# Kernel tuning notes

Hardware: AMD Instinct MI355X
Metric: run time of the kernel (lower is better)

Reference implementation:

```python
import jax, jax.numpy as jnp
import numpy as np

IMG_FEAT = 2048
HIDDEN = 512


def setup_inputs() -> dict:
    key = jax.random.key(0)
    ks = jax.random.split(key, 9)
    B, R = 512, 10
    img = jax.random.normal(ks[0], (B * R, IMG_FEAT), dtype=jnp.float32)
    ques = jax.random.normal(ks[1], (B * R, HIDDEN), dtype=jnp.float32)
    hist = jax.random.normal(ks[2], (B * R, R, HIDDEN), dtype=jnp.float32)
    fusion = IMG_FEAT + HIDDEN
    # kaiming-uniform-ish init scales
    W_fuse = jax.random.uniform(ks[3], (HIDDEN, fusion), dtype=jnp.float32,
                                minval=-1.0, maxval=1.0) * np.sqrt(6.0 / fusion)
    b_fuse = jnp.zeros((HIDDEN,), dtype=jnp.float32)
    w_att = jax.random.uniform(ks[4], (HIDDEN,), dtype=jnp.float32,
                               minval=-1.0, maxval=1.0) * np.sqrt(6.0 / HIDDEN)
    b_att = jnp.zeros((), dtype=jnp.float32)
    W_hist = jax.random.uniform(ks[5], (HIDDEN, HIDDEN), dtype=jnp.float32,
                                minval=-1.0, maxval=1.0) * np.sqrt(6.0 / HIDDEN)
    b_hist = jnp.zeros((HIDDEN,), dtype=jnp.float32)
    return {
        "img": img, "ques": ques, "hist": hist,
        "W_fuse": W_fuse, "b_fuse": b_fuse,
        "w_att": w_att, "b_att": b_att,
        "W_hist": W_hist, "b_hist": b_hist,
        "batch_size": B, "num_rounds": R,
    }


def reference(img, ques, hist, W_fuse, b_fuse, w_att, b_att, W_hist, b_hist,
              batch_size, num_rounds):
    # Dropout is identity (eval mode).
    BR = batch_size * num_rounds
    # fused embedding: tanh(Linear(cat(img, ques)))  -> [B*R, D]
    fused_vec = jnp.concatenate([img, ques], axis=1)
    fused = jnp.tanh(fused_vec @ W_fuse.T + b_fuse)
    D = fused.shape[-1]
    hist_r = hist.reshape(BR, num_rounds, D)  # [B*R, R, D]
    # scores: (hist * broadcast(fused)) @ w_att + b_att  -> [B*R, R]
    # equivalent to the repeat + elementwise-mul + linear-to-scalar in torch
    scores = jnp.einsum('brd,bd,d->br', hist_r, fused, w_att) + b_att
    attn = jax.nn.softmax(scores, axis=1)  # softmax over num_rounds
    hist_embed = jnp.einsum('br,brd->bd', attn, hist_r)  # weighted sum
    hist_embed = jnp.tanh(hist_embed @ W_hist.T + b_hist)
    out = fused + hist_embed
    return out.reshape(batch_size, num_rounds, D)
```

## Files before the change

kernel.cpp:

```cpp
#include <hip/hip_runtime.h>
#include <hip/hip_bf16.h>

#define HIDDEN 512
#define IMGF   2048
#define RNDS   10

typedef float  f32x4  __attribute__((ext_vector_type(4)));
typedef __bf16 bf16x8 __attribute__((ext_vector_type(8)));
typedef unsigned short u16x8 __attribute__((ext_vector_type(8)));

__device__ __forceinline__ unsigned short f2bf(float x) {
    union { float f; unsigned u; } v; v.f = x;
    unsigned r = v.u + 0x7FFFu + ((v.u >> 16) & 1u);
    return (unsigned short)(r >> 16);
}
__device__ __forceinline__ float bf2f(unsigned short h) {
    union { unsigned u; float f; } v; v.u = ((unsigned)h) << 16;
    return v.f;
}

__device__ __forceinline__ void cp16_async(const void* g, void* l) {
    __builtin_amdgcn_global_load_lds(
        (const __attribute__((address_space(1))) unsigned int*)g,
        (__attribute__((address_space(3))) unsigned int*)l,
        16, 0, 0);
}

__global__ __launch_bounds__(256)
void cvt_bf16(const float* __restrict__ p0, long n0,
              const float* __restrict__ p1, long n1,
              const float* __restrict__ p2, long n2,
              const float* __restrict__ p3, long n3,
              unsigned short* __restrict__ q0, unsigned short* __restrict__ q1,
              unsigned short* __restrict__ q2, unsigned short* __restrict__ q3)
{
    long i = ((long)blockIdx.x * 256 + threadIdx.x) * 4;
    const float* s; unsigned short* d; long j;
    if      (i < n0)            { s = p0; d = q0; j = i; }
    else if (i < n0 + n1)       { s = p1; d = q1; j = i - n0; }
    else if (i < n0 + n1 + n2)  { s = p2; d = q2; j = i - n0 - n1; }
    else                        { s = p3; d = q3; j = i - n0 - n1 - n2; }
    float4 v = *(const float4*)(s + j);
    ushort4 o;
    o.x = f2bf(v.x); o.y = f2bf(v.y); o.z = f2bf(v.z); o.w = f2bf(v.w);
    *(ushort4*)(d + j) = o;
}

template<bool RESID>
__global__ __launch_bounds__(256, 4)
void gemm_bt_tanh(const unsigned short* __restrict__ A0, int lda0,
                  const unsigned short* __restrict__ A1, int lda1, int kSplit,
                  const unsigned short* __restrict__ W,
                  const float* __restrict__ bias,
                  const unsigned short* __restrict__ residb,
                  float* __restrict__ outf, unsigned short* __restrict__ outb,
                  int K)
{
    __shared__ unsigned short lA[2][32 * 64];
    __shared__ unsigned short lB[2][64 * 64];

    const int bm = blockIdx.x * 32;
    const int bn = blockIdx.y * 64;
    const int t    = threadIdx.x;
    const int lane = t & 63;
    const int wave = t >> 6;
    const int wm = (wave >> 1) * 16;
    const int wn = (wave & 1) * 32;
    const int lr = lane & 15;
    const int lq = lane >> 4;

    const unsigned short* Wb0 = W + (size_t)bn * K;

    auto stage_tiles = [&](int kt, int buf) {
        int k0 = kt << 6;
        const unsigned short* Ab; int lda;
        if (k0 < kSplit) { Ab = A0 + (size_t)bm * lda0 + k0;            lda = lda0; }
        else             { Ab = A1 + (size_t)bm * lda1 + (k0 - kSplit); lda = lda1; }
        {
            int r = t >> 3, s = (t & 7) ^ (r & 7);
            cp16_async(Ab + (size_t)r * lda + s * 8, &lA[buf][t * 8]);
        }
        #pragma unroll
        for (int h = 0; h < 2; ++h) {
            int ci = h * 256 + t;
            int r = ci >> 3, s = (ci & 7) ^ (r & 7);
            cp16_async(Wb0 + k0 + (size_t)r * K + s * 8, &lB[buf][ci * 8]);
        }
    };

    f32x4 acc[2] = {};
    const int NT = K >> 6;

    stage_tiles(0, 0);
    for (int kt = 0; kt < NT; ++kt) {
        __syncthreads();
        if (kt + 1 < NT) stage_tiles(kt + 1, (kt + 1) & 1);
        const unsigned short* a = &lA[kt & 1][0];
        const unsigned short* b = &lB[kt & 1][0];
        #pragma unroll
        for (int kh = 0; kh < 2; ++kh) {
            const int c = kh * 4 + lq;
            const int ra = wm + lr;
            bf16x8 af = __builtin_bit_cast(bf16x8,
                *(const u16x8*)&a[ra * 64 + ((c ^ (ra & 7)) * 8)]);
            #pragma unroll
            for (int ni = 0; ni < 2; ++ni) {
                const int rb = wn + ni * 16 + lr;
                bf16x8 bf = __builtin_bit_cast(bf16x8,
                    *(const u16x8*)&b[rb * 64 + ((c ^ (rb & 7)) * 8)]);
                acc[ni] = __builtin_amdgcn_mfma_f32_16x16x32_bf16(
                    af, bf, acc[ni], 0, 0, 0);
            }
        }
    }

    #pragma unroll
    for (int ni = 0; ni < 2; ++ni) {
        const int col = bn + wn + ni * 16 + lr;
        const float bc = bias[col];
        const int rbase = bm + wm + lq * 4;
        #pragma unroll
        for (int j = 0; j < 4; ++j) {
            const size_t idx = (size_t)(rbase + j) * HIDDEN + col;
            float v = tanhf(acc[ni][j] + bc);
            if (RESID) outf[idx] = v + bf2f(residb[idx]);
            else       outb[idx] = f2bf(v);
        }
    }
}

__global__ __launch_bounds__(256)
void attn_embed(const float* __restrict__ hist,
                const unsigned short* __restrict__ fusedb,
                const float* __restrict__ w_att,
                const float* __restrict__ b_att,
                unsigned short* __restrict__ hembed)
{
    const int lane = threadIdx.x & 63;
    const int wave = threadIdx.x >> 6;
    const int b = blockIdx.x * 4 + wave;
    const int d = lane * 8;

    float g[8];
    {
        u16x8 f = *(const u16x8*)(fusedb + (size_t)b * HIDDEN + d);
        const float4 w0 = *(const float4*)(w_att + d);
        const float4 w1 = *(const float4*)(w_att + d + 4);
        g[0]=bf2f(f[0])*w0.x; g[1]=bf2f(f[1])*w0.y; g[2]=bf2f(f[2])*w0.z; g[3]=bf2f(f[3])*w0.w;
        g[4]=bf2f(f[4])*w1.x; g[5]=bf2f(f[5])*w1.y; g[6]=bf2f(f[6])*w1.z; g[7]=bf2f(f[7])*w1.w;
    }
    const float* hb = hist + (size_t)b * RNDS * HIDDEN + d;

    float h[RNDS][8], p[RNDS];
    #pragma unroll
    for (int r = 0; r < RNDS; ++r) {
        const float4 a0 = *(const float4*)(hb + r * HIDDEN);
        const float4 a1 = *(const float4*)(hb + r * HIDDEN + 4);
        h[r][0]=a0.x; h[r][1]=a0.y; h[r][2]=a0.z; h[r][3]=a0.w;
        h[r][4]=a1.x; h[r][5]=a1.y; h[r][6]=a1.z; h[r][7]=a1.w;
        float s = 0.f;
        #pragma unroll
        for (int i = 0; i < 8; ++i) s += h[r][i] * g[i];
        p[r] = s;
    }
    #pragma unroll
    for (int r = 0; r < RNDS; ++r)
        #pragma unroll
        for (int m = 1; m < 64; m <<= 1)
            p[r] += __shfl_xor(p[r], m, 64);

    const float ba = b_att[0];
    float mx = -1e30f;
    #pragma unroll
    for (int r = 0; r < RNDS; ++r) mx = fmaxf(mx, p[r] + ba);
    float sum = 0.f, a[RNDS];
    #pragma unroll
    for (int r = 0; r < RNDS; ++r) { a[r] = __expf(p[r] + ba - mx); sum += a[r]; }
    const float inv = 1.0f / sum;

    float e[8] = {};
    #pragma unroll
    for (int r = 0; r < RNDS; ++r)
        #pragma unroll
        for (int i = 0; i < 8; ++i) e[i] += a[r] * h[r][i];

    ushort4 o0, o1;
    o0.x=f2bf(e[0]*inv); o0.y=f2bf(e[1]*inv); o0.z=f2bf(e[2]*inv); o0.w=f2bf(e[3]*inv);
    o1.x=f2bf(e[4]*inv); o1.y=f2bf(e[5]*inv); o1.z=f2bf(e[6]*inv); o1.w=f2bf(e[7]*inv);
    unsigned short* q = hembed + (size_t)b * HIDDEN + d;
    *(ushort4*)q = o0;
    *(ushort4*)(q + 4) = o1;
}

extern "C" void kernel_launch(void* const* d_in, const int* in_sizes, int n_in,
                              void* d_out, int out_size, void* d_ws, size_t ws_size,
                              hipStream_t stream)
{
    const float* img    = (const float*)d_in[0];
    const float* ques   = (const float*)d_in[1];
    const float* hist   = (const float*)d_in[2];
    const float* W_fuse = (const float*)d_in[3];
    const float* b_fuse = (const float*)d_in[4];
    const float* w_att  = (const float*)d_in[5];
    const float* b_att  = (const float*)d_in[6];
    const float* W_hist = (const float*)d_in[7];
    const float* b_hist = (const float*)d_in[8];

    const long n_img  = in_sizes[0];
    const long n_ques = in_sizes[1];
    const long n_Wf   = in_sizes[3];
    const long n_Wh   = in_sizes[7];
    const int  BR     = (int)(n_ques / HIDDEN);

    unsigned short* imgb   = (unsigned short*)d_ws;
    unsigned short* quesb  = imgb   + n_img;
    unsigned short* Wfb    = quesb  + n_ques;
    unsigned short* Whb    = Wfb    + n_Wf;
    unsigned short* fusedb = Whb    + n_Wh;
    unsigned short* hembb  = fusedb + (size_t)BR * HIDDEN;

    const long total4 = (n_img + n_ques + n_Wf + n_Wh) / 4;
    cvt_bf16<<<dim3((unsigned)((total4 + 255) / 256)), dim3(256), 0, stream>>>(
        img, n_img, ques, n_ques, W_fuse, n_Wf, W_hist, n_Wh,
        imgb, quesb, Wfb, Whb);

    dim3 blk(256);
    dim3 g1(BR / 32, HIDDEN / 64);

    gemm_bt_tanh<false><<<g1, blk, 0, stream>>>(
        imgb, IMGF, quesb, HIDDEN, IMGF,
        Wfb, b_fuse, nullptr, nullptr, fusedb, IMGF + HIDDEN);

    attn_embed<<<dim3(BR / 4), blk, 0, stream>>>(hist, fusedb, w_att, b_att, hembb);

    gemm_bt_tanh<true><<<g1, blk, 0, stream>>>(
        hembb, HIDDEN, nullptr, 0, HIDDEN,
        Whb, b_hist, fusedb, (float*)d_out, nullptr, HIDDEN);
}
```

Baseline: 257.0 us.

## Convert activations to bf16 inside GEMM and enlarge tiles with grouped block order

Stops pre-converting img and ques to bf16 in a separate pass. The first GEMM now reads fp32 activations straight from global memory into registers and packs them to bf16 there, with only the weights staged through LDS. Both GEMMs move to 64x64 tiles on 128-thread blocks, with each wave computing 32x64 and a grouped block index intended to improve L2 reuse. This removes a full fp32 read and bf16 write of the activations, but the A operand is now loaded uncached from global per wave, and each block reads it again for every N tile.

```diff
diff --git a/kernel.cpp b/kernel.cpp
--- a/kernel.cpp
+++ b/kernel.cpp
@@ -26,105 +26,184 @@
         16, 0, 0);
 }
 
+__device__ __forceinline__ bf16x8 pack8(float4 p0, float4 p1) {
+    union { bf16x8 v; __hip_bfloat162 h[4]; } u;
+    u.h[0] = __float22bfloat162_rn(make_float2(p0.x, p0.y));
+    u.h[1] = __float22bfloat162_rn(make_float2(p0.z, p0.w));
+    u.h[2] = __float22bfloat162_rn(make_float2(p1.x, p1.y));
+    u.h[3] = __float22bfloat162_rn(make_float2(p1.z, p1.w));
+    return u.v;
+}
+
 __global__ __launch_bounds__(256)
 void cvt_bf16(const float* __restrict__ p0, long n0,
               const float* __restrict__ p1, long n1,
-              const float* __restrict__ p2, long n2,
-              const float* __restrict__ p3, long n3,
-              unsigned short* __restrict__ q0, unsigned short* __restrict__ q1,
-              unsigned short* __restrict__ q2, unsigned short* __restrict__ q3)
+              unsigned short* __restrict__ q0, unsigned short* __restrict__ q1)
 {
     long i = ((long)blockIdx.x * 256 + threadIdx.x) * 4;
     const float* s; unsigned short* d; long j;
-    if      (i < n0)            { s = p0; d = q0; j = i; }
-    else if (i < n0 + n1)       { s = p1; d = q1; j = i - n0; }
-    else if (i < n0 + n1 + n2)  { s = p2; d = q2; j = i - n0 - n1; }
-    else                        { s = p3; d = q3; j = i - n0 - n1 - n2; }
+    if (i < n0) { s = p0; d = q0; j = i; }
+    else        { s = p1; d = q1; j = i - n0; }
     float4 v = *(const float4*)(s + j);
     ushort4 o;
     o.x = f2bf(v.x); o.y = f2bf(v.y); o.z = f2bf(v.z); o.w = f2bf(v.w);
     *(ushort4*)(d + j) = o;
 }
 
-template<bool RESID>
-__global__ __launch_bounds__(256, 4)
-void gemm_bt_tanh(const unsigned short* __restrict__ A0, int lda0,
-                  const unsigned short* __restrict__ A1, int lda1, int kSplit,
-                  const unsigned short* __restrict__ W,
-                  const float* __restrict__ bias,
-                  const unsigned short* __restrict__ residb,
-                  float* __restrict__ outf, unsigned short* __restrict__ outb,
-                  int K)
-{
-    __shared__ unsigned short lA[2][32 * 64];
+__global__ __launch_bounds__(128, 4)
+void gemm1(const float* __restrict__ A0,
+           const float* __restrict__ A1,
+           const unsigned short* __restrict__ W,
+           const float* __restrict__ bias,
+           unsigned short* __restrict__ outb)
+{
     __shared__ unsigned short lB[2][64 * 64];
-
-    const int bm = blockIdx.x * 32;
-    const int bn = blockIdx.y * 64;
+    const int id = blockIdx.x;
+    const int bm = ((id >> 6) * 8 + (id & 7)) * 64;
+    const int bn = ((id >> 3) & 7) * 64;
     const int t    = threadIdx.x;
     const int lane = t & 63;
-    const int wave = t >> 6;
-    const int wm = (wave >> 1) * 16;
-    const int wn = (wave & 1) * 32;
+    const int wv   = t >> 6;
     const int lr = lane & 15;
     const int lq = lane >> 4;
+    const int K = IMGF + HIDDEN;
 
     const unsigned short* Wb0 = W + (size_t)bn * K;
-
-    auto stage_tiles = [&](int kt, int buf) {
+    auto stageB = [&](int kt, int buf) {
         int k0 = kt << 6;
-        const unsigned short* Ab; int lda;
-        if (k0 < kSplit) { Ab = A0 + (size_t)bm * lda0 + k0;            lda = lda0; }
-        else             { Ab = A1 + (size_t)bm * lda1 + (k0 - kSplit); lda = lda1; }
-        {
-            int r = t >> 3, s = (t & 7) ^ (r & 7);
-            cp16_async(Ab + (size_t)r * lda + s * 8, &lA[buf][t * 8]);
-        }
-        #pragma unroll
-        for (int h = 0; h < 2; ++h) {
-            int ci = h * 256 + t;
+        #pragma unroll
+        for (int h = 0; h < 4; ++h) {
+            int ci = h * 128 + t;
             int r = ci >> 3, s = (ci & 7) ^ (r & 7);
             cp16_async(Wb0 + k0 + (size_t)r * K + s * 8, &lB[buf][ci * 8]);
         }
     };
 
-    f32x4 acc[2] = {};
+    const int row0 = bm + wv * 32 + lr;
+    const int row1 = row0 + 16;
+
+    f32x4 acc[2][4] = {};
     const int NT = K >> 6;
 
-    stage_tiles(0, 0);
+    stageB(0, 0);
     for (int kt = 0; kt < NT; ++kt) {
         __syncthreads();
-        if (kt + 1 < NT) stage_tiles(kt + 1, (kt + 1) & 1);
-        const unsigned short* a = &lA[kt & 1][0];
+        if (kt + 1 < NT) stageB(kt + 1, (kt + 1) & 1);
         const unsigned short* b = &lB[kt & 1][0];
+        const int k0 = kt << 6;
+        const float* Ab; int lda, ko;
+        if (k0 < IMGF) { Ab = A0; lda = IMGF;   ko = k0; }
+        else           { Ab = A1; lda = HIDDEN; ko = k0 - IMGF; }
         #pragma unroll
         for (int kh = 0; kh < 2; ++kh) {
-            const int c = kh * 4 + lq;
-            const int ra = wm + lr;
-            bf16x8 af = __builtin_bit_cast(bf16x8,
-                *(const u16x8*)&a[ra * 64 + ((c ^ (ra & 7)) * 8)]);
+            const int kf = ko + kh * 32 + lq * 8;
+            const float* r0p = Ab + (size_t)row0 * lda + kf;
+            const float* r1p = Ab + (size_t)row1 * lda + kf;
+            bf16x8 af[2];
+            af[0] = pack8(*(const float4*)r0p, *(const float4*)(r0p + 4));
+            af[1] = pack8(*(const float4*)r1p, *(const float4*)(r1p + 4));
             #pragma unroll
-            for (int ni = 0; ni < 2; ++ni) {
-                const int rb = wn + ni * 16 + lr;
-                bf16x8 bf = __builtin_bit_cast(bf16x8,
+            for (int ni = 0; ni < 4; ++ni) {
+                const int rb = ni * 16 + lr;
+                const int c  = kh * 4 + lq;
+                bf16x8 bfr = __builtin_bit_cast(bf16x8,
                     *(const u16x8*)&b[rb * 64 + ((c ^ (rb & 7)) * 8)]);
-                acc[ni] = __builtin_amdgcn_mfma_f32_16x16x32_bf16(
-                    af, bf, acc[ni], 0, 0, 0);
+                #pragma unroll
+                for (int mi = 0; mi < 2; ++mi)
+                    acc[mi][ni] = __builtin_amdgcn_mfma_f32_16x16x32_bf16(
+                        af[mi], bfr, acc[mi][ni], 0, 0, 0);
             }
         }
     }
 
     #pragma unroll
-    for (int ni = 0; ni < 2; ++ni) {
-        const int col = bn + wn + ni * 16 + lr;
+    for (int ni = 0; ni < 4; ++ni) {
+        const int col = bn + ni * 16 + lr;
         const float bc = bias[col];
-        const int rbase = bm + wm + lq * 4;
-        #pragma unroll
-        for (int j = 0; j < 4; ++j) {
-            const size_t idx = (size_t)(rbase + j) * HIDDEN + col;
-            float v = tanhf(acc[ni][j] + bc);
-            if (RESID) outf[idx] = v + bf2f(residb[idx]);
-            else       outb[idx] = f2bf(v);
+        #pragma unroll
+        for (int mi = 0; mi < 2; ++mi) {
+            const int rbase = bm + wv * 32 + mi * 16 + lq * 4;
+            #pragma unroll
+            for (int j = 0; j < 4; ++j)
+                outb[(size_t)(rbase + j) * HIDDEN + col] =
+                    f2bf(tanhf(acc[mi][ni][j] + bc));
+        }
+    }
+}
+
+__global__ __launch_bounds__(128, 4)
+void gemm2(const unsigned short* __restrict__ A,
+           const unsigned short* __restrict__ W,
+           const float* __restrict__ bias,
+           const unsigned short* __restrict__ residb,
+           float* __restrict__ outf)
+{
+    __shared__ unsigned short lB[2][64 * 64];
+    const int id = blockIdx.x;
+    const int bm = ((id >> 6) * 8 + (id & 7)) * 64;
+    const int bn = ((id >> 3) & 7) * 64;
+    const int t    = threadIdx.x;
+    const int lane = t & 63;
+    const int wv   = t >> 6;
+    const int lr = lane & 15;
+    const int lq = lane >> 4;
+    const int K = HIDDEN;
+
+    const unsigned short* Wb0 = W + (size_t)bn * K;
+    auto stageB = [&](int kt, int buf) {
+        int k0 = kt << 6;
+        #pragma unroll
+        for (int h = 0; h < 4; ++h) {
+            int ci = h * 128 + t;
+            int r = ci >> 3, s = (ci & 7) ^ (r & 7);
+            cp16_async(Wb0 + k0 + (size_t)r * K + s * 8, &lB[buf][ci * 8]);
+        }
+    };
+
+    const int row0 = bm + wv * 32 + lr;
+    const int row1 = row0 + 16;
+
+    f32x4 acc[2][4] = {};
+    const int NT = K >> 6;
+
+    stageB(0, 0);
+    for (int kt = 0; kt < NT; ++kt) {
+        __syncthreads();
+        if (kt + 1 < NT) stageB(kt + 1, (kt + 1) & 1);
+        const unsigned short* b = &lB[kt & 1][0];
+        const int k0 = kt << 6;
+        #pragma unroll
+        for (int kh = 0; kh < 2; ++kh) {
+            const int kf = k0 + kh * 32 + lq * 8;
+            bf16x8 af[2];
+            af[0] = __builtin_bit_cast(bf16x8, *(const u16x8*)(A + (size_t)row0 * K + kf));
+            af[1] = __builtin_bit_cast(bf16x8, *(const u16x8*)(A + (size_t)row1 * K + kf));
+            #pragma unroll
+            for (int ni = 0; ni < 4; ++ni) {
+                const int rb = ni * 16 + lr;
+                const int c  = kh * 4 + lq;
+                bf16x8 bfr = __builtin_bit_cast(bf16x8,
+                    *(const u16x8*)&b[rb * 64 + ((c ^ (rb & 7)) * 8)]);
+                #pragma unroll
+                for (int mi = 0; mi < 2; ++mi)
+                    acc[mi][ni] = __builtin_amdgcn_mfma_f32_16x16x32_bf16(
+                        af[mi], bfr, acc[mi][ni], 0, 0, 0);
+            }
+        }
+    }
+
+    #pragma unroll
+    for (int ni = 0; ni < 4; ++ni) {
+        const int col = bn + ni * 16 + lr;
+        const float bc = bias[col];
+        #pragma unroll
+        for (int mi = 0; mi < 2; ++mi) {
+            const int rbase = bm + wv * 32 + mi * 16 + lq * 4;
+            #pragma unroll
+            for (int j = 0; j < 4; ++j) {
+                const size_t idx = (size_t)(rbase + j) * HIDDEN + col;
+                outf[idx] = tanhf(acc[mi][ni][j] + bc) + bf2f(residb[idx]);
+            }
         }
     }
 }
@@ -206,34 +285,27 @@
     const float* W_hist = (const float*)d_in[7];
     const float* b_hist = (const float*)d_in[8];
 
-    const long n_img  = in_sizes[0];
-    const long n_ques = in_sizes[1];
-    const long n_Wf   = in_sizes[3];
-    const long n_Wh   = in_sizes[7];
-    const int  BR     = (int)(n_ques / HIDDEN);
-
-    unsigned short* imgb   = (unsigned short*)d_ws;
-    unsigned short* quesb  = imgb   + n_img;
-    unsigned short* Wfb    = quesb  + n_ques;
+    const long n_Wf = in_sizes[3];
+    const long n_Wh = in_sizes[7];
+    const int  BR   = in_sizes[1] / HIDDEN;
+
+    unsigned short* Wfb    = (unsigned short*)d_ws;
     unsigned short* Whb    = Wfb    + n_Wf;
     unsigned short* fusedb = Whb    + n_Wh;
     unsigned short* hembb  = fusedb + (size_t)BR * HIDDEN;
 
-    const long total4 = (n_img + n_ques + n_Wf + n_Wh) / 4;
+    const long total4 = (n_Wf + n_Wh) / 4;
     cvt_bf16<<<dim3((unsigned)((total4 + 255) / 256)), dim3(256), 0, stream>>>(
-        img, n_img, ques, n_ques, W_fuse, n_Wf, W_hist, n_Wh,
-        imgb, quesb, Wfb, Whb);
-
-    dim3 blk(256);
-    dim3 g1(BR / 32, HIDDEN / 64);
-
-    gemm_bt_tanh<false><<<g1, blk, 0, stream>>>(
-        imgb, IMGF, quesb, HIDDEN, IMGF,
-        Wfb, b_fuse, nullptr, nullptr, fusedb, IMGF + HIDDEN);
-
-    attn_embed<<<dim3(BR / 4), blk, 0, stream>>>(hist, fusedb, w_att, b_att, hembb);
-
-    gemm_bt_tanh<true><<<g1, blk, 0, stream>>>(
-        hembb, HIDDEN, nullptr, 0, HIDDEN,
-        Whb, b_hist, fusedb, (float*)d_out, nullptr, HIDDEN);
-}
+        W_fuse, n_Wf, W_hist, n_Wh, Wfb, Whb);
+
+    const int nblk = (BR / 64) * (HIDDEN / 64);
+
+    gemm1<<<dim3(nblk), dim3(128), 0, stream>>>(
+        img, ques, Wfb, b_fuse, fusedb);
+
+    attn_embed<<<dim3(BR / 4), dim3(256), 0, stream>>>(
+        hist, fusedb, w_att, b_att, hembb);
+
+    gemm2<<<dim3(nblk), dim3(128), 0, stream>>>(
+        hembb, Whb, b_hist, fusedb, (float*)d_out);
+}
```

Result: slower. 334.5 us (+30.2%).
